# Kernel optimization log

Hardware: AMD Instinct MI355X
Metric: run time of the kernel (lower is better)

Reference implementation:

```python
import jax, jax.numpy as jnp
import numpy as np

B, E, H, V, T = 64, 512, 1024, 30000, 20
START = 1  # vocab['<start>']


def setup_inputs() -> dict:
    key = jax.random.key(0)
    ks = jax.random.split(key, 12)
    s = 0.05  # small init so log_softmax/tanh stay well-conditioned
    return {
        "encoded_image": jax.random.normal(ks[0], (B, E), jnp.float32),
        "Wemb": jax.random.normal(ks[1], (V, E), jnp.float32) * s,
        "Wih1": jax.random.normal(ks[2], (4 * H, 2 * E), jnp.float32) * s,
        "Whh1": jax.random.normal(ks[3], (4 * H, H), jnp.float32) * s,
        "bih1": jax.random.normal(ks[4], (4 * H,), jnp.float32) * s,
        "bhh1": jax.random.normal(ks[5], (4 * H,), jnp.float32) * s,
        "Wih2": jax.random.normal(ks[6], (4 * H, H), jnp.float32) * s,
        "Whh2": jax.random.normal(ks[7], (4 * H, H), jnp.float32) * s,
        "bih2": jax.random.normal(ks[8], (4 * H,), jnp.float32) * s,
        "bhh2": jax.random.normal(ks[9], (4 * H,), jnp.float32) * s,
        "Wout": jax.random.normal(ks[10], (V, H), jnp.float32) * s,
        "bout": jax.random.normal(ks[11], (V,), jnp.float32) * s,
    }


def _lstm_cell(x, h, c, Wih, Whh, bih, bhh):
    # torch.nn.LSTMCell: gates in (i, f, g, o) row order
    g = x @ Wih.T + bih + h @ Whh.T + bhh
    i, f, gg, o = jnp.split(g, 4, axis=-1)
    c_new = jax.nn.sigmoid(f) * c + jax.nn.sigmoid(i) * jnp.tanh(gg)
    h_new = jax.nn.sigmoid(o) * jnp.tanh(c_new)
    return h_new, c_new


def reference(encoded_image, Wemb, Wih1, Whh1, bih1, bhh1,
              Wih2, Whh2, bih2, bhh2, Wout, bout):
    Bn = encoded_image.shape[0]
    dt = encoded_image.dtype
    h1 = c1 = h2 = c2 = jnp.zeros((Bn, H), dt)
    # pre-loop step with zero word embedding
    x0 = jnp.concatenate([encoded_image, jnp.zeros((Bn, E), dt)], axis=-1)
    h1, c1 = _lstm_cell(x0, h1, c1, Wih1, Whh1, bih1, bhh1)
    h2, c2 = _lstm_cell(h1, h2, c2, Wih2, Whh2, bih2, bhh2)
    # output[:, 0] = one_hot(<start>)  (dropout is identity in eval mode)
    row0 = jnp.zeros((Bn, V), dt).at[:, START].set(1.0)
    prev_tok = jnp.full((Bn,), START, jnp.int32)

    def step(carry, _):
        h1, c1, h2, c2, tok = carry
        emb = Wemb[tok]                                   # [B, E] gather
        x = jnp.concatenate([encoded_image, emb], axis=-1)
        h1, c1 = _lstm_cell(x, h1, c1, Wih1, Whh1, bih1, bhh1)
        h2, c2 = _lstm_cell(h1, h2, c2, Wih2, Whh2, bih2, bhh2)
        logp = jax.nn.log_softmax(h2 @ Wout.T + bout, axis=-1)  # [B, V]
        tok = jnp.argmax(logp, axis=-1).astype(jnp.int32)
        return (h1, c1, h2, c2, tok), logp

    _, rows = jax.lax.scan(step, (h1, c1, h2, c2, prev_tok), None, length=T - 1)
    out = jnp.concatenate([row0[:, None, :], jnp.transpose(rows, (1, 0, 2))], axis=1)
    return out  # [B, T, V]
```

## Files before the change

### kernel.cpp

```cpp
#include <hip/hip_runtime.h>
#include <math.h>

#define BB 64
#define EE 512
#define HH 1024
#define VV 30000
#define TT 20
#define NBT 469
#define PSTRIDE 512

typedef __attribute__((ext_vector_type(8))) short bf16x8;
typedef __attribute__((ext_vector_type(4))) float f32x4;

#define OFF_W1  ((size_t)0)
#define OFF_W2  ((size_t)33554432)
#define OFF_WO  ((size_t)67108864)
#define OFF_X1  ((size_t)190054400)
#define OFF_H1  ((size_t)190316544)
#define OFF_H2  ((size_t)190840832)
#define OFF_C1  ((size_t)191365120)
#define OFF_C2  ((size_t)191627264)
#define OFF_P   ((size_t)191889408)
#define OFF_PM  ((size_t)196083712)
#define OFF_PS  ((size_t)196214784)
#define OFF_PA  ((size_t)196345856)
#define OFF_LSE ((size_t)196476928)
#define OFF_BS  ((size_t)196482048)

__device__ __forceinline__ unsigned short bf_hi(float x) {
    unsigned u = __float_as_uint(x);
    return (unsigned short)((u + 0x7fffu + ((u >> 16) & 1u)) >> 16);
}
__device__ __forceinline__ float bf_f(unsigned short h) {
    return __uint_as_float(((unsigned)h) << 16);
}
__device__ __forceinline__ void merge3(float& m, float& s, int& a,
                                       float m2, float s2, int a2) {
    if (m2 > m) { s = s * expf(m - m2) + s2; m = m2; a = a2; }
    else if (m2 == m) { s += s2; if (a2 < a) a = a2; }
    else { s += s2 * expf(m2 - m); }
}
__device__ __forceinline__ void gl16(const void* g, void* l) {
    __builtin_amdgcn_global_load_lds(
        (const unsigned int __attribute__((address_space(1)))*)g,
        (unsigned int __attribute__((address_space(3)))*)l, 16, 0, 0);
}
__device__ __forceinline__ void cvt8(const float* src, uint4& hv, uint4& lv) {
    unsigned h[8], q[8];
    #pragma unroll
    for (int i = 0; i < 8; ++i) {
        float x = src[i];
        unsigned short hi = bf_hi(x);
        unsigned short lo = bf_hi(x - bf_f(hi));
        h[i] = hi; q[i] = lo;
    }
    hv.x = h[0] | (h[1] << 16); hv.y = h[2] | (h[3] << 16);
    hv.z = h[4] | (h[5] << 16); hv.w = h[6] | (h[7] << 16);
    lv.x = q[0] | (q[1] << 16); lv.y = q[2] | (q[3] << 16);
    lv.z = q[4] | (q[5] << 16); lv.w = q[6] | (q[7] << 16);
}

__global__ __launch_bounds__(256) void k_conv_cell(
    const float* __restrict__ Wih1, const float* __restrict__ Whh1,
    const float* __restrict__ Wih2, const float* __restrict__ Whh2, char* wsb) {
    int cell = blockIdx.y;
    const float* Wih = cell ? Wih2 : Wih1;
    const float* Whh = cell ? Whh2 : Whh1;
    char* dst = wsb + (cell ? OFF_W2 : OFF_W1);
    unsigned flat = blockIdx.x * 256 + threadIdx.x;
    unsigned c = flat & 511, kt = (flat >> 9) & 31, rt = flat >> 14;
    unsigned s = c >> 8, bg = (c >> 6) & 3, g = (c >> 4) & 3, n = c & 15;
    unsigned row = bg * 1024 + rt * 16 + n;
    unsigned col = (kt & 15) * 64 + s * 32 + g * 8;
    const float* src = (kt < 16 ? Wih : Whh) + (size_t)row * 1024 + col;
    uint4 hv, lv; cvt8(src, hv, lv);
    char* d = dst + (size_t)rt * 524288 + kt * 16384 + c * 16;
    *(uint4*)d = hv;
    *(uint4*)(d + 8192) = lv;
}

__global__ __launch_bounds__(256) void k_conv_out(const float* __restrict__ Wout,
                                                  char* wsb) {
    unsigned flat = blockIdx.x * 256 + threadIdx.x;
    unsigned c = flat & 511, kt = (flat >> 9) & 15, rt = flat >> 13;
    unsigned s = c >> 8, bg = (c >> 6) & 3, g = (c >> 4) & 3, n = c & 15;
    unsigned row = rt * 64 + bg * 16 + n; if (row > VV - 1) row = VV - 1;
    unsigned col = kt * 64 + s * 32 + g * 8;
    const float* src = Wout + (size_t)row * 1024 + col;
    uint4 hv, lv; cvt8(src, hv, lv);
    char* d = wsb + OFF_WO + (size_t)rt * 262144 + kt * 16384 + c * 16;
    *(uint4*)d = hv;
    *(uint4*)(d + 8192) = lv;
}

__global__ __launch_bounds__(256) void k_conv_img(const float* __restrict__ img,
                                                  char* wsb) {
    unsigned flat = blockIdx.x * 256 + threadIdx.x;
    unsigned c = flat & 511, kt = flat >> 9;
    unsigned s = c >> 8, bg = (c >> 6) & 3, g = (c >> 4) & 3, n = c & 15;
    unsigned b = bg * 16 + n;
    unsigned col = kt * 64 + s * 32 + g * 8;
    const float* src = img + (size_t)b * 512 + col;
    uint4 hv, lv; cvt8(src, hv, lv);
    char* d = wsb + OFF_X1 + kt * 16384 + c * 16;
    *(uint4*)d = hv;
    *(uint4*)(d + 8192) = lv;
}

__global__ void k_prep(char* wsb,
                       const float* __restrict__ bih1, const float* __restrict__ bhh1,
                       const float* __restrict__ bih2, const float* __restrict__ bhh2) {
    unsigned idx = blockIdx.x * 256 + threadIdx.x;
    if (idx < 131072) { ((unsigned*)(wsb + OFF_C1))[idx] = 0u; return; }
    idx -= 131072;
    if (idx < 65536) { ((unsigned*)(wsb + OFF_H1))[idx] = 0u; return; }
    idx -= 65536;
    if (idx < 65536) { ((unsigned*)(wsb + OFF_H2))[idx] = 0u; return; }
    idx -= 65536;
    if (idx < 32768) { ((unsigned*)(wsb + OFF_X1 + 131072))[idx] = 0u; return; }
    idx -= 32768;
    if (idx < 8192) {
        float v = (idx < 4096) ? bih1[idx] + bhh1[idx]
                               : bih2[idx - 4096] + bhh2[idx - 4096];
        ((float*)(wsb + OFF_BS))[idx] = v;
    }
}

__device__ __forceinline__ void emb_write(char* X1, const float* Wemb, int tk,
                                          int b, int tid) {
    #pragma unroll
    for (int i = 0; i < 2; ++i) {
        int e = tid + i * 256;
        float x = Wemb[(size_t)tk * 512 + e];
        unsigned short hi = bf_hi(x);
        unsigned short lo = bf_hi(x - bf_f(hi));
        int k = 512 + e;
        int kt = k >> 6, kl = k & 63;
        int s = kl >> 5, gq = (kl >> 3) & 3, off = kl & 7;
        int chunk = s * 256 + (b >> 4) * 64 + gq * 16 + (b & 15);
        char* d = X1 + kt * 16384 + chunk * 16 + off * 2;
        *(unsigned short*)d = hi;
        *(unsigned short*)(d + 8192) = lo;
    }
}

__global__ void k_emb0(const float* __restrict__ Wemb, char* wsb) {
    emb_write(wsb + OFF_X1, Wemb, 1, blockIdx.x, threadIdx.x);
}

template <int NKT>
__device__ __forceinline__ void gemm_core(const char* __restrict__ Wsrc,
                                          const char* __restrict__ Asrc,
                                          char* smem, int tid, f32x4 acc[4]) {
    const int l = tid & 63, w = tid >> 6, g = l >> 4, n = l & 15;
    auto stage = [&](int kt, char* buf) {
        const char* wsp = Wsrc + kt * 16384;
        const char* asp = Asrc + kt * 16384;
        int o = tid * 16;
        gl16(wsp + o, buf + o);
        gl16(wsp + 4096 + o, buf + 4096 + o);
        gl16(wsp + 8192 + o, buf + 8192 + o);
        gl16(wsp + 12288 + o, buf + 12288 + o);
        gl16(asp + o, buf + 16384 + o);
        gl16(asp + 4096 + o, buf + 20480 + o);
        gl16(asp + 8192 + o, buf + 24576 + o);
        gl16(asp + 12288 + o, buf + 28672 + o);
    };
    stage(0, smem);
    __syncthreads();
    for (int kt = 0; kt < NKT; ++kt) {
        char* buf = smem + (kt & 1) * 32768;
        if (kt + 1 < NKT) stage(kt + 1, smem + ((kt + 1) & 1) * 32768);
        #pragma unroll
        for (int s = 0; s < 2; ++s) {
            int wc = (s * 256 + w * 64 + g * 16 + n) * 16;
            bf16x8 ah = *(const bf16x8*)(buf + wc);
            bf16x8 al = *(const bf16x8*)(buf + 8192 + wc);
            #pragma unroll
            for (int bg = 0; bg < 4; ++bg) {
                int ac = (s * 256 + bg * 64 + g * 16 + n) * 16;
                bf16x8 bh = *(const bf16x8*)(buf + 16384 + ac);
                bf16x8 bl = *(const bf16x8*)(buf + 24576 + ac);
                acc[bg] = __builtin_amdgcn_mfma_f32_16x16x32_bf16(ah, bh, acc[bg], 0, 0, 0);
                acc[bg] = __builtin_amdgcn_mfma_f32_16x16x32_bf16(ah, bl, acc[bg], 0, 0, 0);
                acc[bg] = __builtin_amdgcn_mfma_f32_16x16x32_bf16(al, bh, acc[bg], 0, 0, 0);
            }
        }
        __syncthreads();
    }
}

__global__ __launch_bounds__(256) void k_cellg(const char* __restrict__ Wbase,
                                               const char* __restrict__ Ax,
                                               const char* __restrict__ Ah,
                                               float* __restrict__ P) {
    __shared__ __align__(16) char smem[65536];
    const int tid = threadIdx.x;
    const int rt = blockIdx.x & 63, kq = blockIdx.x >> 6;
    const char* Wsrc = Wbase + (size_t)rt * 524288 + kq * 131072;
    const char* Asrc = (kq < 2) ? Ax + kq * 131072 : Ah + (kq - 2) * 131072;
    f32x4 acc[4];
    #pragma unroll
    for (int i = 0; i < 4; ++i) acc[i] = (f32x4){0.f, 0.f, 0.f, 0.f};
    gemm_core<8>(Wsrc, Asrc, smem, tid, acc);
    const int l = tid & 63, w = tid >> 6, g = l >> 4, n = l & 15;
    float* Pd = P + kq * 262144 + rt * 4096;
    #pragma unroll
    for (int bg = 0; bg < 4; ++bg)
        #pragma unroll
        for (int p = 0; p < 4; ++p)
            Pd[(w * 16 + g * 4 + p) * 64 + bg * 16 + n] = acc[bg][p];
}

__global__ void k_act(const float* __restrict__ P, const float* __restrict__ bs,
                      float* __restrict__ c, char* __restrict__ Hdst) {
    int rt = blockIdx.x, bq = blockIdx.y;
    int jl = threadIdx.x >> 4, bl = threadIdx.x & 15;
    int b = bq * 16 + bl;
    int base = rt * 4096;
    float g4[4];
    #pragma unroll
    for (int gg = 0; gg < 4; ++gg) {
        float v = 0.f;
        #pragma unroll
        for (int kq = 0; kq < 4; ++kq)
            v += P[kq * 262144 + base + (gg * 16 + jl) * 64 + b];
        g4[gg] = v + bs[gg * 1024 + rt * 16 + jl];
    }
    float si = 1.f / (1.f + expf(-g4[0]));
    float sf = 1.f / (1.f + expf(-g4[1]));
    float so = 1.f / (1.f + expf(-g4[3]));
    float tg = tanhf(g4[2]);
    int j = rt * 16 + jl;
    int ci = b * 1024 + j;
    float cn = sf * c[ci] + si * tg;
    c[ci] = cn;
    float hn = so * tanhf(cn);
    unsigned short hi = bf_hi(hn);
    unsigned short lo = bf_hi(hn - bf_f(hi));
    int kt = j >> 6, kl = j & 63;
    int s = kl >> 5, gq = (kl >> 3) & 3, off = kl & 7;
    int chunk = s * 256 + (b >> 4) * 64 + gq * 16 + (b & 15);
    char* d = Hdst + kt * 16384 + chunk * 16 + off * 2;
    *(unsigned short*)d = hi;
    *(unsigned short*)(d + 8192) = lo;
}

__global__ __launch_bounds__(256) void k_logits(
    const char* __restrict__ WObase, const float* __restrict__ bout,
    const char* __restrict__ A, float* __restrict__ out, int tstep,
    float* __restrict__ pm, float* __restrict__ ps, int* __restrict__ pa) {
    __shared__ __align__(16) char smem[65536];
    const int tid = threadIdx.x;
    const int v0 = blockIdx.x * 64;
    const char* Wsrc = WObase + (size_t)blockIdx.x * 262144;
    f32x4 acc[4];
    #pragma unroll
    for (int i = 0; i < 4; ++i) acc[i] = (f32x4){0.f, 0.f, 0.f, 0.f};
    gemm_core<16>(Wsrc, A, smem, tid, acc);
    const int l = tid & 63, w = tid >> 6, g = l >> 4, n = l & 15;
    int bidx = v0 + w * 16 + g * 4; if (bidx > VV - 4) bidx = VV - 4;
    f32x4 bb4 = *(const f32x4*)&bout[bidx];
    float* gl = (float*)smem;
    #pragma unroll
    for (int bg = 0; bg < 4; ++bg)
        #pragma unroll
        for (int p = 0; p < 4; ++p)
            gl[(bg * 16 + n) * 68 + w * 16 + g * 4 + p] = acc[bg][p] + bb4[p];
    __syncthreads();
    int b = tid >> 2, vq = tid & 3;
    float m = -INFINITY, ssum = 0.f; int am = VV;
    if (v0 + vq * 16 < VV) {
        size_t ob = ((size_t)b * TT + tstep) * VV + v0 + vq * 16;
        #pragma unroll
        for (int e4 = 0; e4 < 4; ++e4) {
            f32x4 vv = *(const f32x4*)&gl[b * 68 + vq * 16 + e4 * 4];
            *(f32x4*)&out[ob + e4 * 4] = vv;
            #pragma unroll
            for (int p = 0; p < 4; ++p)
                merge3(m, ssum, am, vv[p], 1.f, v0 + vq * 16 + e4 * 4 + p);
        }
    }
    #pragma unroll
    for (int off = 1; off < 4; off <<= 1) {
        float m2 = __shfl_xor(m, off, 64);
        float s2 = __shfl_xor(ssum, off, 64);
        int a2 = __shfl_xor(am, off, 64);
        merge3(m, ssum, am, m2, s2, a2);
    }
    if (vq == 0) {
        pm[b * PSTRIDE + blockIdx.x] = m;
        ps[b * PSTRIDE + blockIdx.x] = ssum;
        pa[b * PSTRIDE + blockIdx.x] = am;
    }
}

__global__ void k_reduce(const float* __restrict__ pm, const float* __restrict__ ps,
                         const int* __restrict__ pa, float* __restrict__ lse_all,
                         int t, const float* __restrict__ Wemb, char* __restrict__ X1) {
    int b = blockIdx.x;
    int tid = threadIdx.x;
    float m = -INFINITY, s = 0.f; int a = VV;
    for (int i = tid; i < NBT; i += 256)
        merge3(m, s, a, pm[(size_t)b * PSTRIDE + i], ps[(size_t)b * PSTRIDE + i],
               pa[(size_t)b * PSTRIDE + i]);
    #pragma unroll
    for (int off = 1; off < 64; off <<= 1) {
        float m2 = __shfl_xor(m, off, 64);
        float s2 = __shfl_xor(s, off, 64);
        int   a2 = __shfl_xor(a, off, 64);
        merge3(m, s, a, m2, s2, a2);
    }
    __shared__ float sm[4], ss[4]; __shared__ int sa[4]; __shared__ int stok;
    if ((tid & 63) == 0) { sm[tid >> 6] = m; ss[tid >> 6] = s; sa[tid >> 6] = a; }
    __syncthreads();
    if (tid == 0) {
        for (int w = 1; w < 4; ++w) merge3(m, s, a, sm[w], ss[w], sa[w]);
        lse_all[t * 64 + b] = m + logf(s);
        stok = a;
    }
    __syncthreads();
    emb_write(X1, Wemb, stok, b, tid);
}

__global__ void k_fix(float* __restrict__ out, const float* __restrict__ lse_all) {
    int v = blockIdx.x * 256 + threadIdx.x;
    int t = blockIdx.y, b = blockIdx.z;
    if (v >= VV) return;
    size_t o = ((size_t)b * TT + t) * VV + v;
    if (t == 0) out[o] = (v == 1) ? 1.f : 0.f;
    else out[o] -= lse_all[t * 64 + b];
}

extern "C" void kernel_launch(void* const* d_in, const int* in_sizes, int n_in,
                              void* d_out, int out_size, void* d_ws, size_t ws_size,
                              hipStream_t stream) {
    const float* img   = (const float*)d_in[0];
    const float* Wemb  = (const float*)d_in[1];
    const float* Wih1  = (const float*)d_in[2];
    const float* Whh1  = (const float*)d_in[3];
    const float* bih1  = (const float*)d_in[4];
    const float* bhh1  = (const float*)d_in[5];
    const float* Wih2  = (const float*)d_in[6];
    const float* Whh2  = (const float*)d_in[7];
    const float* bih2  = (const float*)d_in[8];
    const float* bhh2  = (const float*)d_in[9];
    const float* Wout  = (const float*)d_in[10];
    const float* bout  = (const float*)d_in[11];
    float* out = (float*)d_out;
    char*  wsb = (char*)d_ws;

    char* W1 = wsb + OFF_W1;
    char* W2 = wsb + OFF_W2;
    char* WO = wsb + OFF_WO;
    char* X1 = wsb + OFF_X1;
    float* c1 = (float*)(wsb + OFF_C1);
    float* c2 = (float*)(wsb + OFF_C2);
    float* P  = (float*)(wsb + OFF_P);
    float* pm = (float*)(wsb + OFF_PM);
    float* ps = (float*)(wsb + OFF_PS);
    int*   pa = (int*)(wsb + OFF_PA);
    float* lse_all = (float*)(wsb + OFF_LSE);
    float* bs = (float*)(wsb + OFF_BS);
    auto Hb = [&](size_t base, int bank) { return wsb + base + (size_t)bank * 262144; };

    k_conv_cell<<<dim3(4096, 2), 256, 0, stream>>>(Wih1, Whh1, Wih2, Whh2, wsb);
    k_conv_out<<<15008, 256, 0, stream>>>(Wout, wsb);
    k_conv_img<<<16, 256, 0, stream>>>(img, wsb);
    k_prep<<<1184, 256, 0, stream>>>(wsb, bih1, bhh1, bih2, bhh2);

    int cur = 0;
    k_cellg<<<256, 256, 0, stream>>>(W1, X1, Hb(OFF_H1, cur), P);
    k_emb0<<<64, 256, 0, stream>>>(Wemb, wsb);
    k_act<<<dim3(64, 4), 256, 0, stream>>>(P, bs, c1, Hb(OFF_H1, cur ^ 1));
    k_cellg<<<256, 256, 0, stream>>>(W2, Hb(OFF_H1, cur ^ 1), Hb(OFF_H2, cur), P);
    k_act<<<dim3(64, 4), 256, 0, stream>>>(P, bs + 4096, c2, Hb(OFF_H2, cur ^ 1));
    cur = 1;

    for (int t = 1; t < TT; ++t) {
        k_cellg<<<256, 256, 0, stream>>>(W1, X1, Hb(OFF_H1, cur), P);
        k_act<<<dim3(64, 4), 256, 0, stream>>>(P, bs, c1, Hb(OFF_H1, cur ^ 1));
        k_cellg<<<256, 256, 0, stream>>>(W2, Hb(OFF_H1, cur ^ 1), Hb(OFF_H2, cur), P);
        k_act<<<dim3(64, 4), 256, 0, stream>>>(P, bs + 4096, c2, Hb(OFF_H2, cur ^ 1));
        k_logits<<<NBT, 256, 0, stream>>>(WO, bout, Hb(OFF_H2, cur ^ 1),
                                          out, t, pm, ps, pa);
        k_reduce<<<64, 256, 0, stream>>>(pm, ps, pa, lse_all, t, Wemb, X1);
        cur ^= 1;
    }
    k_fix<<<dim3(118, TT, BB), 256, 0, stream>>>(out, lse_all);
}
```

Before: 1.269 ms.

## Precompute loop-invariant image gate contribution and halve GEMM staging buffers

The encoded_image part of the layer-1 input projection is the same at every step. It is now computed once by a new kernel (k_gximg), with the bias folded in, and added in k_act, so the per-step layer-1 GEMM covers only the embedding and recurrent K ranges (6 tiles per quarter instead of 8). gemm_core now stages half k-tiles into 32KB of LDS instead of 64KB, which may raise occupancy but doubles the number of barriers. k_logits writes its output with nontemporal stores, and k_fix is vectorised to float4 with nontemporal load and store.

Result: slower. 1.469 ms (+15.8%).

```diff
diff --git a/kernel.cpp b/kernel.cpp
--- a/kernel.cpp
+++ b/kernel.cpp
@@ -26,6 +26,7 @@
 #define OFF_PA  ((size_t)196345856)
 #define OFF_LSE ((size_t)196476928)
 #define OFF_BS  ((size_t)196482048)
+#define OFF_GX  ((size_t)196515840)
 
 __device__ __forceinline__ unsigned short bf_hi(float x) {
     unsigned u = __float_as_uint(x);
@@ -148,61 +149,79 @@
     emb_write(wsb + OFF_X1, Wemb, 1, blockIdx.x, threadIdx.x);
 }
 
-template <int NKT>
+template <int NU>
 __device__ __forceinline__ void gemm_core(const char* __restrict__ Wsrc,
-                                          const char* __restrict__ Asrc,
+                                          const char* __restrict__ A0,
+                                          const char* __restrict__ A1,
+                                          int ktbase, int HALF,
                                           char* smem, int tid, f32x4 acc[4]) {
     const int l = tid & 63, w = tid >> 6, g = l >> 4, n = l & 15;
-    auto stage = [&](int kt, char* buf) {
-        const char* wsp = Wsrc + kt * 16384;
-        const char* asp = Asrc + kt * 16384;
+    auto stage = [&](int u, char* buf) {
+        int t = u >> 1, s = u & 1;
+        const char* wsp = Wsrc + t * 16384 + s * 4096;
+        int ta = ktbase + t;
+        const char* a0 = (ta < HALF) ? (A0 + ta * 16384) : (A1 + (ta - HALF) * 16384);
+        const char* asp = a0 + s * 4096;
         int o = tid * 16;
         gl16(wsp + o, buf + o);
-        gl16(wsp + 4096 + o, buf + 4096 + o);
-        gl16(wsp + 8192 + o, buf + 8192 + o);
-        gl16(wsp + 12288 + o, buf + 12288 + o);
-        gl16(asp + o, buf + 16384 + o);
-        gl16(asp + 4096 + o, buf + 20480 + o);
-        gl16(asp + 8192 + o, buf + 24576 + o);
-        gl16(asp + 12288 + o, buf + 28672 + o);
+        gl16(wsp + 8192 + o, buf + 4096 + o);
+        gl16(asp + o, buf + 8192 + o);
+        gl16(asp + 8192 + o, buf + 12288 + o);
     };
     stage(0, smem);
     __syncthreads();
-    for (int kt = 0; kt < NKT; ++kt) {
-        char* buf = smem + (kt & 1) * 32768;
-        if (kt + 1 < NKT) stage(kt + 1, smem + ((kt + 1) & 1) * 32768);
-        #pragma unroll
-        for (int s = 0; s < 2; ++s) {
-            int wc = (s * 256 + w * 64 + g * 16 + n) * 16;
-            bf16x8 ah = *(const bf16x8*)(buf + wc);
-            bf16x8 al = *(const bf16x8*)(buf + 8192 + wc);
-            #pragma unroll
-            for (int bg = 0; bg < 4; ++bg) {
-                int ac = (s * 256 + bg * 64 + g * 16 + n) * 16;
-                bf16x8 bh = *(const bf16x8*)(buf + 16384 + ac);
-                bf16x8 bl = *(const bf16x8*)(buf + 24576 + ac);
-                acc[bg] = __builtin_amdgcn_mfma_f32_16x16x32_bf16(ah, bh, acc[bg], 0, 0, 0);
-                acc[bg] = __builtin_amdgcn_mfma_f32_16x16x32_bf16(ah, bl, acc[bg], 0, 0, 0);
-                acc[bg] = __builtin_amdgcn_mfma_f32_16x16x32_bf16(al, bh, acc[bg], 0, 0, 0);
-            }
+    const int wc = (w * 64 + g * 16 + n) * 16;
+    for (int u = 0; u < NU; ++u) {
+        char* buf = smem + (u & 1) * 16384;
+        if (u + 1 < NU) stage(u + 1, smem + ((u + 1) & 1) * 16384);
+        bf16x8 ah = *(const bf16x8*)(buf + wc);
+        bf16x8 al = *(const bf16x8*)(buf + 4096 + wc);
+        #pragma unroll
+        for (int bg = 0; bg < 4; ++bg) {
+            int ac = (bg * 64 + g * 16 + n) * 16;
+            bf16x8 bh = *(const bf16x8*)(buf + 8192 + ac);
+            bf16x8 bl = *(const bf16x8*)(buf + 12288 + ac);
+            acc[bg] = __builtin_amdgcn_mfma_f32_16x16x32_bf16(ah, bh, acc[bg], 0, 0, 0);
+            acc[bg] = __builtin_amdgcn_mfma_f32_16x16x32_bf16(ah, bl, acc[bg], 0, 0, 0);
+            acc[bg] = __builtin_amdgcn_mfma_f32_16x16x32_bf16(al, bh, acc[bg], 0, 0, 0);
         }
         __syncthreads();
     }
 }
 
+__global__ __launch_bounds__(256) void k_gximg(char* wsb) {
+    __shared__ __align__(16) char smem[32768];
+    const int cid = blockIdx.x, tid = threadIdx.x;
+    const int l = tid & 63, w = tid >> 6, g = l >> 4, n = l & 15;
+    f32x4 acc[4];
+    #pragma unroll
+    for (int i = 0; i < 4; ++i) acc[i] = (f32x4){0.f, 0.f, 0.f, 0.f};
+    gemm_core<16>(wsb + OFF_W1 + (size_t)cid * 524288,
+                  wsb + OFF_X1, wsb + OFF_X1, 0, 16, smem, tid, acc);
+    const float* bs = (const float*)(wsb + OFF_BS);
+    float* gx = (float*)(wsb + OFF_GX) + cid * 4096;
+    #pragma unroll
+    for (int bg = 0; bg < 4; ++bg)
+        #pragma unroll
+        for (int p = 0; p < 4; ++p)
+            gx[(w * 16 + g * 4 + p) * 64 + bg * 16 + n] =
+                acc[bg][p] + bs[w * 1024 + cid * 16 + g * 4 + p];
+}
+
+template <int KQT>
 __global__ __launch_bounds__(256) void k_cellg(const char* __restrict__ Wbase,
-                                               const char* __restrict__ Ax,
-                                               const char* __restrict__ Ah,
-                                               float* __restrict__ P) {
-    __shared__ __align__(16) char smem[65536];
+                                               size_t Wskip,
+                                               const char* __restrict__ A0,
+                                               const char* __restrict__ A1,
+                                               int HALF, float* __restrict__ P) {
+    __shared__ __align__(16) char smem[32768];
     const int tid = threadIdx.x;
     const int rt = blockIdx.x & 63, kq = blockIdx.x >> 6;
-    const char* Wsrc = Wbase + (size_t)rt * 524288 + kq * 131072;
-    const char* Asrc = (kq < 2) ? Ax + kq * 131072 : Ah + (kq - 2) * 131072;
+    const char* Wsrc = Wbase + (size_t)rt * 524288 + Wskip + (size_t)kq * KQT * 16384;
     f32x4 acc[4];
     #pragma unroll
     for (int i = 0; i < 4; ++i) acc[i] = (f32x4){0.f, 0.f, 0.f, 0.f};
-    gemm_core<8>(Wsrc, Asrc, smem, tid, acc);
+    gemm_core<2 * KQT>(Wsrc, A0, A1, kq * KQT, HALF, smem, tid, acc);
     const int l = tid & 63, w = tid >> 6, g = l >> 4, n = l & 15;
     float* Pd = P + kq * 262144 + rt * 4096;
     #pragma unroll
@@ -213,6 +232,7 @@
 }
 
 __global__ void k_act(const float* __restrict__ P, const float* __restrict__ bs,
+                      const float* __restrict__ gx,
                       float* __restrict__ c, char* __restrict__ Hdst) {
     int rt = blockIdx.x, bq = blockIdx.y;
     int jl = threadIdx.x >> 4, bl = threadIdx.x & 15;
@@ -225,7 +245,8 @@
         #pragma unroll
         for (int kq = 0; kq < 4; ++kq)
             v += P[kq * 262144 + base + (gg * 16 + jl) * 64 + b];
-        g4[gg] = v + bs[gg * 1024 + rt * 16 + jl];
+        g4[gg] = v + (gx ? gx[rt * 4096 + gg * 1024 + jl * 64 + b]
+                         : bs[gg * 1024 + rt * 16 + jl]);
     }
     float si = 1.f / (1.f + expf(-g4[0]));
     float sf = 1.f / (1.f + expf(-g4[1]));
@@ -250,18 +271,19 @@
     const char* __restrict__ WObase, const float* __restrict__ bout,
     const char* __restrict__ A, float* __restrict__ out, int tstep,
     float* __restrict__ pm, float* __restrict__ ps, int* __restrict__ pa) {
-    __shared__ __align__(16) char smem[65536];
+    __shared__ __align__(16) char smem[32768];
     const int tid = threadIdx.x;
     const int v0 = blockIdx.x * 64;
     const char* Wsrc = WObase + (size_t)blockIdx.x * 262144;
     f32x4 acc[4];
     #pragma unroll
     for (int i = 0; i < 4; ++i) acc[i] = (f32x4){0.f, 0.f, 0.f, 0.f};
-    gemm_core<16>(Wsrc, A, smem, tid, acc);
+    gemm_core<32>(Wsrc, A, A, 0, 16, smem, tid, acc);
     const int l = tid & 63, w = tid >> 6, g = l >> 4, n = l & 15;
     int bidx = v0 + w * 16 + g * 4; if (bidx > VV - 4) bidx = VV - 4;
     f32x4 bb4 = *(const f32x4*)&bout[bidx];
     float* gl = (float*)smem;
+    __syncthreads();
     #pragma unroll
     for (int bg = 0; bg < 4; ++bg)
         #pragma unroll
@@ -275,7 +297,7 @@
         #pragma unroll
         for (int e4 = 0; e4 < 4; ++e4) {
             f32x4 vv = *(const f32x4*)&gl[b * 68 + vq * 16 + e4 * 4];
-            *(f32x4*)&out[ob + e4 * 4] = vv;
+            __builtin_nontemporal_store(vv, (f32x4*)&out[ob + e4 * 4]);
             #pragma unroll
             for (int p = 0; p < 4; ++p)
                 merge3(m, ssum, am, vv[p], 1.f, v0 + vq * 16 + e4 * 4 + p);
@@ -324,12 +346,20 @@
 }
 
 __global__ void k_fix(float* __restrict__ out, const float* __restrict__ lse_all) {
-    int v = blockIdx.x * 256 + threadIdx.x;
+    int v4 = blockIdx.x * 256 + threadIdx.x;
     int t = blockIdx.y, b = blockIdx.z;
-    if (v >= VV) return;
-    size_t o = ((size_t)b * TT + t) * VV + v;
-    if (t == 0) out[o] = (v == 1) ? 1.f : 0.f;
-    else out[o] -= lse_all[t * 64 + b];
+    if (v4 >= 7500) return;
+    size_t o = ((size_t)b * TT + t) * VV + (size_t)v4 * 4;
+    f32x4 vv;
+    if (t == 0) {
+        vv = (f32x4){0.f, 0.f, 0.f, 0.f};
+        if (v4 == 0) vv[1] = 1.f;
+    } else {
+        vv = __builtin_nontemporal_load((const f32x4*)&out[o]);
+        float lz = lse_all[t * 64 + b];
+        vv[0] -= lz; vv[1] -= lz; vv[2] -= lz; vv[3] -= lz;
+    }
+    __builtin_nontemporal_store(vv, (f32x4*)&out[o]);
 }
 
 extern "C" void kernel_launch(void* const* d_in, const int* in_sizes, int n_in,
@@ -362,30 +392,38 @@
     int*   pa = (int*)(wsb + OFF_PA);
     float* lse_all = (float*)(wsb + OFF_LSE);
     float* bs = (float*)(wsb + OFF_BS);
+    float* gx = (float*)(wsb + OFF_GX);
     auto Hb = [&](size_t base, int bank) { return wsb + base + (size_t)bank * 262144; };
 
     k_conv_cell<<<dim3(4096, 2), 256, 0, stream>>>(Wih1, Whh1, Wih2, Whh2, wsb);
     k_conv_out<<<15008, 256, 0, stream>>>(Wout, wsb);
     k_conv_img<<<16, 256, 0, stream>>>(img, wsb);
     k_prep<<<1184, 256, 0, stream>>>(wsb, bih1, bhh1, bih2, bhh2);
+    k_gximg<<<64, 256, 0, stream>>>(wsb);
 
     int cur = 0;
-    k_cellg<<<256, 256, 0, stream>>>(W1, X1, Hb(OFF_H1, cur), P);
+    k_cellg<6><<<256, 256, 0, stream>>>(W1, 131072, X1 + 131072, Hb(OFF_H1, cur),
+                                        8, P);
     k_emb0<<<64, 256, 0, stream>>>(Wemb, wsb);
-    k_act<<<dim3(64, 4), 256, 0, stream>>>(P, bs, c1, Hb(OFF_H1, cur ^ 1));
-    k_cellg<<<256, 256, 0, stream>>>(W2, Hb(OFF_H1, cur ^ 1), Hb(OFF_H2, cur), P);
-    k_act<<<dim3(64, 4), 256, 0, stream>>>(P, bs + 4096, c2, Hb(OFF_H2, cur ^ 1));
+    k_act<<<dim3(64, 4), 256, 0, stream>>>(P, bs, gx, c1, Hb(OFF_H1, cur ^ 1));
+    k_cellg<8><<<256, 256, 0, stream>>>(W2, 0, Hb(OFF_H1, cur ^ 1), Hb(OFF_H2, cur),
+                                        16, P);
+    k_act<<<dim3(64, 4), 256, 0, stream>>>(P, bs + 4096, nullptr, c2,
+                                           Hb(OFF_H2, cur ^ 1));
     cur = 1;
 
     for (int t = 1; t < TT; ++t) {
-        k_cellg<<<256, 256, 0, stream>>>(W1, X1, Hb(OFF_H1, cur), P);
-        k_act<<<dim3(64, 4), 256, 0, stream>>>(P, bs, c1, Hb(OFF_H1, cur ^ 1));
-        k_cellg<<<256, 256, 0, stream>>>(W2, Hb(OFF_H1, cur ^ 1), Hb(OFF_H2, cur), P);
-        k_act<<<dim3(64, 4), 256, 0, stream>>>(P, bs + 4096, c2, Hb(OFF_H2, cur ^ 1));
+        k_cellg<6><<<256, 256, 0, stream>>>(W1, 131072, X1 + 131072, Hb(OFF_H1, cur),
+                                            8, P);
+        k_act<<<dim3(64, 4), 256, 0, stream>>>(P, bs, gx, c1, Hb(OFF_H1, cur ^ 1));
+        k_cellg<8><<<256, 256, 0, stream>>>(W2, 0, Hb(OFF_H1, cur ^ 1),
+                                            Hb(OFF_H2, cur), 16, P);
+        k_act<<<dim3(64, 4), 256, 0, stream>>>(P, bs + 4096, nullptr, c2,
+                                               Hb(OFF_H2, cur ^ 1));
         k_logits<<<NBT, 256, 0, stream>>>(WO, bout, Hb(OFF_H2, cur ^ 1),
                                           out, t, pm, ps, pa);
         k_reduce<<<64, 256, 0, stream>>>(pm, ps, pa, lse_all, t, Wemb, X1);
         cur ^= 1;
     }
-    k_fix<<<dim3(118, TT, BB), 256, 0, stream>>>(out, lse_all);
-}
+    k_fix<<<dim3(30, TT, BB), 256, 0, stream>>>(out, lse_all);
+}
```

## Hoist image-input gate GEMM out of loop and fuse LSTM activation into cell GEMM

Applied to the files above, without the earlier changes.

Precomputes the image part of the layer-1 input projection once (k_gximg, bias folded in), so each step's layer-1 GEMM covers only the embedding and hidden columns. The split-K cell GEMM plus separate activation kernel is merged into one kernel per layer that reduces the full K in a block and applies the LSTM nonlinearities from LDS. This removes the partial-sum buffer round trip and two launches per step. The trade-off is only 64 blocks per cell GEMM instead of 256, each with a longer K loop, which may leave many CUs idle. Logit stores become nontemporal and the final fix-up kernel is vectorized to float4.

New measurement: 1.850 ms. 1.46x slower.

```diff
diff --git a/kernel.cpp b/kernel.cpp
--- a/kernel.cpp
+++ b/kernel.cpp
@@ -20,12 +20,12 @@
 #define OFF_H2  ((size_t)190840832)
 #define OFF_C1  ((size_t)191365120)
 #define OFF_C2  ((size_t)191627264)
-#define OFF_P   ((size_t)191889408)
 #define OFF_PM  ((size_t)196083712)
 #define OFF_PS  ((size_t)196214784)
 #define OFF_PA  ((size_t)196345856)
 #define OFF_LSE ((size_t)196476928)
 #define OFF_BS  ((size_t)196482048)
+#define OFF_GX  ((size_t)196515840)
 
 __device__ __forceinline__ unsigned short bf_hi(float x) {
     unsigned u = __float_as_uint(x);
@@ -150,12 +150,15 @@
 
 template <int NKT>
 __device__ __forceinline__ void gemm_core(const char* __restrict__ Wsrc,
-                                          const char* __restrict__ Asrc,
+                                          const char* __restrict__ A0,
+                                          const char* __restrict__ A1,
+                                          int HALF,
                                           char* smem, int tid, f32x4 acc[4]) {
     const int l = tid & 63, w = tid >> 6, g = l >> 4, n = l & 15;
     auto stage = [&](int kt, char* buf) {
         const char* wsp = Wsrc + kt * 16384;
-        const char* asp = Asrc + kt * 16384;
+        const char* asp = (kt < HALF) ? (A0 + kt * 16384)
+                                      : (A1 + (kt - HALF) * 16384);
         int o = tid * 16;
         gl16(wsp + o, buf + o);
         gl16(wsp + 4096 + o, buf + 4096 + o);
@@ -190,60 +193,86 @@
     }
 }
 
-__global__ __launch_bounds__(256) void k_cellg(const char* __restrict__ Wbase,
-                                               const char* __restrict__ Ax,
-                                               const char* __restrict__ Ah,
-                                               float* __restrict__ P) {
+__global__ __launch_bounds__(256) void k_gximg(char* wsb) {
     __shared__ __align__(16) char smem[65536];
-    const int tid = threadIdx.x;
-    const int rt = blockIdx.x & 63, kq = blockIdx.x >> 6;
-    const char* Wsrc = Wbase + (size_t)rt * 524288 + kq * 131072;
-    const char* Asrc = (kq < 2) ? Ax + kq * 131072 : Ah + (kq - 2) * 131072;
+    const int cid = blockIdx.x, tid = threadIdx.x;
+    const int l = tid & 63, w = tid >> 6, g = l >> 4, n = l & 15;
     f32x4 acc[4];
     #pragma unroll
     for (int i = 0; i < 4; ++i) acc[i] = (f32x4){0.f, 0.f, 0.f, 0.f};
-    gemm_core<8>(Wsrc, Asrc, smem, tid, acc);
-    const int l = tid & 63, w = tid >> 6, g = l >> 4, n = l & 15;
-    float* Pd = P + kq * 262144 + rt * 4096;
+    gemm_core<8>(wsb + OFF_W1 + (size_t)cid * 524288,
+                 wsb + OFF_X1, wsb + OFF_X1, 8, smem, tid, acc);
+    const float* bs = (const float*)(wsb + OFF_BS);
+    float* gx = (float*)(wsb + OFF_GX) + cid * 4096;
     #pragma unroll
     for (int bg = 0; bg < 4; ++bg)
         #pragma unroll
         for (int p = 0; p < 4; ++p)
-            Pd[(w * 16 + g * 4 + p) * 64 + bg * 16 + n] = acc[bg][p];
-}
-
-__global__ void k_act(const float* __restrict__ P, const float* __restrict__ bs,
-                      float* __restrict__ c, char* __restrict__ Hdst) {
-    int rt = blockIdx.x, bq = blockIdx.y;
-    int jl = threadIdx.x >> 4, bl = threadIdx.x & 15;
-    int b = bq * 16 + bl;
-    int base = rt * 4096;
-    float g4[4];
-    #pragma unroll
-    for (int gg = 0; gg < 4; ++gg) {
-        float v = 0.f;
+            gx[(w * 16 + g * 4 + p) * 64 + bg * 16 + n] =
+                acc[bg][p] + bs[w * 1024 + cid * 16 + g * 4 + p];
+}
+
+template <int NKT>
+__global__ __launch_bounds__(256) void k_cell(const char* __restrict__ Wbase,
+                                              size_t Wskip,
+                                              const char* __restrict__ A0,
+                                              const char* __restrict__ A1, int HALF,
+                                              const float* __restrict__ bsc,
+                                              const float* __restrict__ gx,
+                                              float* __restrict__ cc,
+                                              char* __restrict__ Hd) {
+    __shared__ __align__(16) char smem[65536];
+    const int tid = threadIdx.x, rt = blockIdx.x;
+    const int l = tid & 63, w = tid >> 6, g = l >> 4, n = l & 15;
+    f32x4 acc[4];
+    #pragma unroll
+    for (int i = 0; i < 4; ++i) acc[i] = (f32x4){0.f, 0.f, 0.f, 0.f};
+    gemm_core<NKT>(Wbase + (size_t)rt * 524288 + Wskip, A0, A1, HALF,
+                   smem, tid, acc);
+    float* glc = (float*)smem;
+    #pragma unroll
+    for (int bg = 0; bg < 4; ++bg)
         #pragma unroll
-        for (int kq = 0; kq < 4; ++kq)
-            v += P[kq * 262144 + base + (gg * 16 + jl) * 64 + b];
-        g4[gg] = v + bs[gg * 1024 + rt * 16 + jl];
-    }
-    float si = 1.f / (1.f + expf(-g4[0]));
-    float sf = 1.f / (1.f + expf(-g4[1]));
-    float so = 1.f / (1.f + expf(-g4[3]));
-    float tg = tanhf(g4[2]);
-    int j = rt * 16 + jl;
-    int ci = b * 1024 + j;
-    float cn = sf * c[ci] + si * tg;
-    c[ci] = cn;
-    float hn = so * tanhf(cn);
-    unsigned short hi = bf_hi(hn);
-    unsigned short lo = bf_hi(hn - bf_f(hi));
-    int kt = j >> 6, kl = j & 63;
-    int s = kl >> 5, gq = (kl >> 3) & 3, off = kl & 7;
-    int chunk = s * 256 + (b >> 4) * 64 + gq * 16 + (b & 15);
-    char* d = Hdst + kt * 16384 + chunk * 16 + off * 2;
-    *(unsigned short*)d = hi;
-    *(unsigned short*)(d + 8192) = lo;
+        for (int p = 0; p < 4; ++p)
+            glc[w * 1024 + (g * 4 + p) * 64 + bg * 16 + n] = acc[bg][p];
+    __syncthreads();
+    #pragma unroll
+    for (int i = 0; i < 4; ++i) {
+        int e = tid + 256 * i;
+        int b = e & 63, jo = e >> 6;
+        float a0, a1, a2, a3;
+        if (gx) {
+            a0 = gx[rt * 4096 + jo * 64 + b];
+            a1 = gx[rt * 4096 + 1024 + jo * 64 + b];
+            a2 = gx[rt * 4096 + 2048 + jo * 64 + b];
+            a3 = gx[rt * 4096 + 3072 + jo * 64 + b];
+        } else {
+            a0 = bsc[rt * 16 + jo];
+            a1 = bsc[1024 + rt * 16 + jo];
+            a2 = bsc[2048 + rt * 16 + jo];
+            a3 = bsc[3072 + rt * 16 + jo];
+        }
+        float gi = glc[jo * 64 + b]        + a0;
+        float gf = glc[1024 + jo * 64 + b] + a1;
+        float gg = glc[2048 + jo * 64 + b] + a2;
+        float go = glc[3072 + jo * 64 + b] + a3;
+        float si = 1.f / (1.f + expf(-gi));
+        float sf = 1.f / (1.f + expf(-gf));
+        float so = 1.f / (1.f + expf(-go));
+        int j = rt * 16 + jo;
+        int ci = b * 1024 + j;
+        float cn = sf * cc[ci] + si * tanhf(gg);
+        cc[ci] = cn;
+        float hn = so * tanhf(cn);
+        unsigned short hi = bf_hi(hn);
+        unsigned short lo = bf_hi(hn - bf_f(hi));
+        int kt = j >> 6, kl = j & 63;
+        int s = kl >> 5, gq = (kl >> 3) & 3, off = kl & 7;
+        int chunk = s * 256 + (b >> 4) * 64 + gq * 16 + (b & 15);
+        char* d = Hd + kt * 16384 + chunk * 16 + off * 2;
+        *(unsigned short*)d = hi;
+        *(unsigned short*)(d + 8192) = lo;
+    }
 }
 
 __global__ __launch_bounds__(256) void k_logits(
@@ -257,7 +286,7 @@
     f32x4 acc[4];
     #pragma unroll
     for (int i = 0; i < 4; ++i) acc[i] = (f32x4){0.f, 0.f, 0.f, 0.f};
-    gemm_core<16>(Wsrc, A, smem, tid, acc);
+    gemm_core<16>(Wsrc, A, A, 16, smem, tid, acc);
     const int l = tid & 63, w = tid >> 6, g = l >> 4, n = l & 15;
     int bidx = v0 + w * 16 + g * 4; if (bidx > VV - 4) bidx = VV - 4;
     f32x4 bb4 = *(const f32x4*)&bout[bidx];
@@ -275,7 +304,7 @@
         #pragma unroll
         for (int e4 = 0; e4 < 4; ++e4) {
             f32x4 vv = *(const f32x4*)&gl[b * 68 + vq * 16 + e4 * 4];
-            *(f32x4*)&out[ob + e4 * 4] = vv;
+            __builtin_nontemporal_store(vv, (f32x4*)&out[ob + e4 * 4]);
             #pragma unroll
             for (int p = 0; p < 4; ++p)
                 merge3(m, ssum, am, vv[p], 1.f, v0 + vq * 16 + e4 * 4 + p);
@@ -324,12 +353,20 @@
 }
 
 __global__ void k_fix(float* __restrict__ out, const float* __restrict__ lse_all) {
-    int v = blockIdx.x * 256 + threadIdx.x;
+    int v4 = blockIdx.x * 256 + threadIdx.x;
     int t = blockIdx.y, b = blockIdx.z;
-    if (v >= VV) return;
-    size_t o = ((size_t)b * TT + t) * VV + v;
-    if (t == 0) out[o] = (v == 1) ? 1.f : 0.f;
-    else out[o] -= lse_all[t * 64 + b];
+    if (v4 >= 7500) return;
+    size_t o = ((size_t)b * TT + t) * VV + (size_t)v4 * 4;
+    f32x4 vv;
+    if (t == 0) {
+        vv = (f32x4){0.f, 0.f, 0.f, 0.f};
+        if (v4 == 0) vv[1] = 1.f;
+    } else {
+        vv = *(const f32x4*)&out[o];
+        float lz = lse_all[t * 64 + b];
+        vv[0] -= lz; vv[1] -= lz; vv[2] -= lz; vv[3] -= lz;
+    }
+    *(f32x4*)&out[o] = vv;
 }
 
 extern "C" void kernel_launch(void* const* d_in, const int* in_sizes, int n_in,
@@ -356,36 +393,38 @@
     char* X1 = wsb + OFF_X1;
     float* c1 = (float*)(wsb + OFF_C1);
     float* c2 = (float*)(wsb + OFF_C2);
-    float* P  = (float*)(wsb + OFF_P);
     float* pm = (float*)(wsb + OFF_PM);
     float* ps = (float*)(wsb + OFF_PS);
     int*   pa = (int*)(wsb + OFF_PA);
     float* lse_all = (float*)(wsb + OFF_LSE);
     float* bs = (float*)(wsb + OFF_BS);
+    float* gx = (float*)(wsb + OFF_GX);
     auto Hb = [&](size_t base, int bank) { return wsb + base + (size_t)bank * 262144; };
 
     k_conv_cell<<<dim3(4096, 2), 256, 0, stream>>>(Wih1, Whh1, Wih2, Whh2, wsb);
     k_conv_out<<<15008, 256, 0, stream>>>(Wout, wsb);
     k_conv_img<<<16, 256, 0, stream>>>(img, wsb);
     k_prep<<<1184, 256, 0, stream>>>(wsb, bih1, bhh1, bih2, bhh2);
+    k_gximg<<<64, 256, 0, stream>>>(wsb);
 
     int cur = 0;
-    k_cellg<<<256, 256, 0, stream>>>(W1, X1, Hb(OFF_H1, cur), P);
+    k_cell<24><<<64, 256, 0, stream>>>(W1, 131072, X1 + 131072, Hb(OFF_H1, cur), 8,
+                                       bs, gx, c1, Hb(OFF_H1, cur ^ 1));
     k_emb0<<<64, 256, 0, stream>>>(Wemb, wsb);
-    k_act<<<dim3(64, 4), 256, 0, stream>>>(P, bs, c1, Hb(OFF_H1, cur ^ 1));
-    k_cellg<<<256, 256, 0, stream>>>(W2, Hb(OFF_H1, cur ^ 1), Hb(OFF_H2, cur), P);
-    k_act<<<dim3(64, 4), 256, 0, stream>>>(P, bs + 4096, c2, Hb(OFF_H2, cur ^ 1));
+    k_cell<32><<<64, 256, 0, stream>>>(W2, 0, Hb(OFF_H1, cur ^ 1), Hb(OFF_H2, cur), 16,
+                                       bs + 4096, nullptr, c2, Hb(OFF_H2, cur ^ 1));
     cur = 1;
 
     for (int t = 1; t < TT; ++t) {
-        k_cellg<<<256, 256, 0, stream>>>(W1, X1, Hb(OFF_H1, cur), P);
-        k_act<<<dim3(64, 4), 256, 0, stream>>>(P, bs, c1, Hb(OFF_H1, cur ^ 1));
-        k_cellg<<<256, 256, 0, stream>>>(W2, Hb(OFF_H1, cur ^ 1), Hb(OFF_H2, cur), P);
-        k_act<<<dim3(64, 4), 256, 0, stream>>>(P, bs + 4096, c2, Hb(OFF_H2, cur ^ 1));
+        k_cell<24><<<64, 256, 0, stream>>>(W1, 131072, X1 + 131072, Hb(OFF_H1, cur), 8,
+                                           bs, gx, c1, Hb(OFF_H1, cur ^ 1));
+        k_cell<32><<<64, 256, 0, stream>>>(W2, 0, Hb(OFF_H1, cur ^ 1),
+                                           Hb(OFF_H2, cur), 16,
+                                           bs + 4096, nullptr, c2, Hb(OFF_H2, cur ^ 1));
         k_logits<<<NBT, 256, 0, stream>>>(WO, bout, Hb(OFF_H2, cur ^ 1),
                                           out, t, pm, ps, pa);
         k_reduce<<<64, 256, 0, stream>>>(pm, ps, pa, lse_all, t, Wemb, X1);
         cur ^= 1;
     }
-    k_fix<<<dim3(118, TT, BB), 256, 0, stream>>>(out, lse_all);
-}
+    k_fix<<<dim3(30, TT, BB), 256, 0, stream>>>(out, lse_all);
+}
```
